# Performance work log

Hardware: AMD Instinct MI355X
Metric: run time of the kernel (lower is better)

## Reference

```python
import jax, jax.numpy as jnp
import numpy as np

B, S, H, N, NREL = 16, 2048, 1024, 128, 8


def setup_inputs() -> dict:
    key = jax.random.key(0)
    ks = jax.random.split(key, 8)
    word_emb = jax.random.normal(ks[0], (B, S, H), dtype=jnp.float32)
    num_ids = jax.random.randint(ks[1], (B, N), 0, S)  # all valid (no -1 padding)
    is_response = jax.random.randint(ks[2], (B, N), 0, 2).astype(jnp.int32)
    numbers = jax.random.normal(ks[3], (B, N), dtype=jnp.float32)
    scale = 1.0 / np.sqrt(H).astype(np.float32)
    w_alpha = jax.random.normal(ks[4], (H, 1), dtype=jnp.float32) * scale
    b_alpha = jnp.zeros((1,), dtype=jnp.float32)
    w_f = jax.random.normal(ks[5], (H, H), dtype=jnp.float32) * scale
    b_f = jnp.zeros((H,), dtype=jnp.float32)
    W_r = jax.random.normal(ks[6], (NREL, H, H), dtype=jnp.float32) * scale  # 8 bias-free relation linears
    return dict(word_emb=word_emb, num_ids=num_ids, is_response=is_response,
                numbers=numbers, w_alpha=w_alpha, b_alpha=b_alpha,
                w_f=w_f, b_f=b_f, W_r=W_r)


def reference(word_emb, num_ids, is_response, numbers, w_alpha, b_alpha, w_f, b_f, W_r):
    Bn, Sn, Hn = word_emb.shape
    Nn = num_ids.shape[1]
    mask = (num_ids >= 0)  # [B,N] valid-node mask (original uses -1 padding)
    idx = jnp.clip(num_ids, 0, Sn - 1)
    # per-batch gather: Init[b,n] = word_emb[b, num_ids[b,n]]  -> [B,N,H]
    Init = jnp.take_along_axis(word_emb, idx[:, :, None], axis=1)
    alpha = jax.nn.sigmoid(Init @ w_alpha + b_alpha)  # [B,N,1]
    # all 8 relation transforms of every sender node j: T[b,r,j,:] = Init[b,j] @ W_r[r].T
    T = jnp.einsum('bnh,rkh->brnk', Init, W_r)  # [B,8,N,H]
    # relation id r(b,i,j) = 4*(num_i>num_j) + 2*resp_i + resp_j
    gt = (numbers[:, :, None] > numbers[:, None, :]).astype(jnp.int32)  # [B,N,N]
    resp = (is_response == 1).astype(jnp.int32)
    R = 4 * gt + 2 * resp[:, :, None] + resp[:, None, :]  # [B,N,N]
    sel = jax.nn.one_hot(R, NREL, dtype=word_emb.dtype)  # [B,N,N,8]
    not_diag = ~jnp.eye(Nn, dtype=bool)
    # edge weight over sender j: alpha_j, valid i & j, i != j
    wgt = (alpha[:, None, :, 0] * mask[:, None, :] * mask[:, :, None]
           * not_diag[None]).astype(word_emb.dtype)  # [B,N,N]
    Temp = jnp.einsum('bijr,brjh->bih', sel * wgt[..., None], T)  # [B,N,H]
    n_nodes = mask.sum(axis=1)  # [B]
    denom = jnp.maximum(n_nodes - 1, 1).astype(word_emb.dtype)
    Temp = Temp / denom[:, None, None]
    out = jax.nn.relu(Init @ w_f + b_f + Temp)  # [B,N,H]
    return out
```

## Files before the change

kernel.cpp:

```cpp
#include <hip/hip_runtime.h>
#include <hip/hip_bf16.h>
#include <stdint.h>

#define B_ 16
#define S_ 2048
#define H_ 1024
#define N_ 128
#define K9 (9*H_)
#define M_ (B_*N_)

typedef __attribute__((ext_vector_type(8))) short s8vec;
typedef __attribute__((ext_vector_type(4))) float f4vec;
typedef __hip_bfloat16 bf16;

__global__ void k_sort(const int* __restrict__ num_ids, const int* __restrict__ is_resp,
                       const float* __restrict__ numbers,
                       int* __restrict__ sigma, int* __restrict__ newgrp,
                       int* __restrict__ respv, float* __restrict__ denom) {
    int b = blockIdx.x, i = threadIdx.x;
    __shared__ float nums[N_];
    __shared__ int sig[N_];
    __shared__ int cnt;
    float ni = numbers[b*N_ + i];
    int idv = num_ids[b*N_ + i];
    int valid = (idv >= 0) ? 1 : 0;
    nums[i] = ni;
    if (i == 0) cnt = 0;
    __syncthreads();
    int p = 0;
    for (int j = 0; j < N_; ++j) {
        float nj = nums[j];
        p += (nj < ni || (nj == ni && j < i)) ? 1 : 0;
    }
    sig[p] = i;
    atomicAdd(&cnt, valid);
    __syncthreads();
    sigma[b*N_ + i] = sig[i];
    int cur = sig[i];
    int prv = (i > 0) ? sig[i-1] : 0;
    newgrp[b*N_ + i] = (i == 0 || nums[cur] != nums[prv]) ? 1 : 0;
    respv[b*N_ + i] = ((is_resp[b*N_ + i] == 1) ? 1 : 0) | (valid << 1);
    if (i == 0) denom[b] = fmaxf((float)(cnt - 1), 1.0f);
}

__global__ void k_gather(const float* __restrict__ word_emb, const int* __restrict__ num_ids,
                         const float* __restrict__ w_alpha, const float* __restrict__ b_alpha,
                         const float* __restrict__ denom,
                         bf16* __restrict__ A, float* __restrict__ ascaled) {
    int blk = blockIdx.x;
    int b = blk >> 7, n = blk & 127;
    int t = threadIdx.x;
    int idv = num_ids[b*N_ + n];
    int valid = (idv >= 0) ? 1 : 0;
    int idx = idv < 0 ? 0 : (idv > S_-1 ? S_-1 : idv);
    const float4* row = (const float4*)(word_emb + ((size_t)b*S_ + idx)*H_);
    float4 v = row[t];
    float4 w = ((const float4*)w_alpha)[t];
    float part = v.x*w.x + v.y*w.y + v.z*w.z + v.w*w.w;
    bf16* dst = A + (size_t)(b*N_ + n)*K9 + 8*H_ + t*4;
    dst[0] = __float2bfloat16(v.x);
    dst[1] = __float2bfloat16(v.y);
    dst[2] = __float2bfloat16(v.z);
    dst[3] = __float2bfloat16(v.w);
#pragma unroll
    for (int off = 32; off > 0; off >>= 1) part += __shfl_down(part, off, 64);
    __shared__ float red[4];
    if ((t & 63) == 0) red[t >> 6] = part;
    __syncthreads();
    if (t == 0) {
        float dot = red[0] + red[1] + red[2] + red[3] + b_alpha[0];
        float al = 1.0f / (1.0f + __expf(-dot));
        ascaled[b*N_ + n] = valid ? (al / denom[b]) : 0.0f;
    }
}

__global__ void k_wt(const float* __restrict__ W_r, bf16* __restrict__ Wt) {
    size_t o = ((size_t)blockIdx.x*256 + threadIdx.x)*4;
    float4 v = *(const float4*)(W_r + o);
    Wt[o+0] = __float2bfloat16(v.x);
    Wt[o+1] = __float2bfloat16(v.y);
    Wt[o+2] = __float2bfloat16(v.z);
    Wt[o+3] = __float2bfloat16(v.w);
}

__global__ void k_wf(const float* __restrict__ w_f, bf16* __restrict__ Wt8) {
    __shared__ float lds[64][65];
    int bi = blockIdx.x, bj = blockIdx.y;
    int t = threadIdx.x;
    int ty = t >> 4, tx = t & 15;
#pragma unroll
    for (int i = 0; i < 4; ++i) {
        int r = ty*4 + i;
        float4 v = *(const float4*)(w_f + (size_t)(bi*64 + r)*H_ + bj*64 + tx*4);
        lds[r][tx*4+0] = v.x; lds[r][tx*4+1] = v.y;
        lds[r][tx*4+2] = v.z; lds[r][tx*4+3] = v.w;
    }
    __syncthreads();
#pragma unroll
    for (int i = 0; i < 4; ++i) {
        int n = ty*4 + i;
        bf16* dst = Wt8 + (size_t)(bj*64 + n)*H_ + bi*64 + tx*4;
#pragma unroll
        for (int j = 0; j < 4; ++j)
            dst[j] = __float2bfloat16(lds[tx*4+j][n]);
    }
}

__global__ void k_build(const float* __restrict__ ascaled, const int* __restrict__ sigma,
                        const int* __restrict__ newgrp, const int* __restrict__ respv,
                        bf16* __restrict__ A) {
    int b = blockIdx.y;
    int h = blockIdx.x*64 + threadIdx.x;
    __shared__ float as_s[N_];
    __shared__ int sig_s[N_], ng_s[N_], rv_s[N_];
    for (int j = threadIdx.x; j < N_; j += 64) {
        as_s[j] = ascaled[b*N_ + j];
        sig_s[j] = sigma[b*N_ + j];
        ng_s[j] = newgrp[b*N_ + j];
        rv_s[j] = respv[b*N_ + j];
    }
    __syncthreads();
    const bf16* initcol = A + 8*H_ + h;
    float tot0 = 0.f, tot1 = 0.f;
    for (int i2 = 0; i2 < N_; ++i2) {
        float v = as_s[i2] * __bfloat162float(initcol[(size_t)(b*N_ + i2)*K9]);
        if (rv_s[i2] & 1) tot1 += v; else tot0 += v;
    }
    float cS0=0.f, cS1=0.f, cG0=0.f, cG1=0.f;
    for (int p = 0; p < N_; ++p) {
        int i2 = sig_s[p];
        if (ng_s[p]) { cS0 += cG0; cS1 += cG1; cG0 = 0.f; cG1 = 0.f; }
        float v = as_s[i2] * __bfloat162float(initcol[(size_t)(b*N_ + i2)*K9]);
        int resp = rv_s[i2] & 1;
        float vf = (rv_s[i2] >> 1) ? 1.0f : 0.0f;
        float G0 = cS0, G1 = cS1;
        float L0 = tot0 - G0 - (resp ? 0.f : v);
        float L1 = tot1 - G1 - (resp ? v : 0.f);
        bf16* Ar = A + (size_t)(b*N_ + i2)*K9 + h;
        int rb = 2*resp, ob = 2*(1 - resp);
        Ar[(size_t)(rb+0)*H_]   = __float2bfloat16(L0*vf);
        Ar[(size_t)(rb+1)*H_]   = __float2bfloat16(L1*vf);
        Ar[(size_t)(4+rb+0)*H_] = __float2bfloat16(G0*vf);
        Ar[(size_t)(4+rb+1)*H_] = __float2bfloat16(G1*vf);
        bf16 z = __float2bfloat16(0.0f);
        Ar[(size_t)(ob+0)*H_]   = z;
        Ar[(size_t)(ob+1)*H_]   = z;
        Ar[(size_t)(4+ob+0)*H_] = z;
        Ar[(size_t)(4+ob+1)*H_] = z;
        if (resp) cG1 += v; else cG0 += v;
    }
}

#define BM 128
#define BN 128
#define BK 32
#define KSPLIT 4
#define KSEG (K9/KSPLIT)

__global__ __launch_bounds__(256) void k_gemm(const bf16* __restrict__ A,
                                              const bf16* __restrict__ Wt,
                                              float* __restrict__ out) {
    __shared__ __align__(16) bf16 As[BM*BK];
    __shared__ __align__(16) bf16 Bs[BN*BK];
    int tid = threadIdx.x;
    int w = tid >> 6, lane = tid & 63;
    int q = lane >> 4, r = lane & 15;
    int bid = blockIdx.x;
    int mtile = bid & 15, ntile = (bid >> 4) & 7, ks = bid >> 7;
    int rowBase = mtile * BM, colBase = ntile * BN;
    int wm = w >> 1, wn = w & 1;

    f4vec acc[4][4];
#pragma unroll
    for (int mt = 0; mt < 4; ++mt)
#pragma unroll
        for (int nt = 0; nt < 4; ++nt)
#pragma unroll
            for (int e = 0; e < 4; ++e) acc[mt][nt][e] = 0.0f;

    const size_t Abase = (size_t)rowBase * K9;
    const int kbeg = ks * KSEG, kend = kbeg + KSEG;
    for (int k0 = kbeg; k0 < kend; k0 += BK) {
        int slot = k0 >> 10, kin = k0 & 1023;
        {
            int c = tid;
            const bf16* g = A + Abase + (size_t)(c & 127)*K9 + k0 + (c >> 7)*8;
            __builtin_amdgcn_global_load_lds((const __attribute__((address_space(1))) void*)g,
                (__attribute__((address_space(3))) void*)((char*)As + w*1024), 16, 0, 0);
            c = tid + 256;
            const bf16* g2 = A + Abase + (size_t)(c & 127)*K9 + k0 + (c >> 7)*8;
            __builtin_amdgcn_global_load_lds((const __attribute__((address_space(1))) void*)g2,
                (__attribute__((address_space(3))) void*)((char*)As + 4096 + w*1024), 16, 0, 0);
            c = tid;
            const bf16* gb = Wt + (size_t)slot*H_*H_ + (size_t)(colBase + (c & 127))*H_
                             + kin + (c >> 7)*8;
            __builtin_amdgcn_global_load_lds((const __attribute__((address_space(1))) void*)gb,
                (__attribute__((address_space(3))) void*)((char*)Bs + w*1024), 16, 0, 0);
            c = tid + 256;
            const bf16* gb2 = Wt + (size_t)slot*H_*H_ + (size_t)(colBase + (c & 127))*H_
                              + kin + (c >> 7)*8;
            __builtin_amdgcn_global_load_lds((const __attribute__((address_space(1))) void*)gb2,
                (__attribute__((address_space(3))) void*)((char*)Bs + 4096 + w*1024), 16, 0, 0);
        }
        __syncthreads();
        const short* Asp = (const short*)As;
        const short* Bsp = (const short*)Bs;
        s8vec af[4], bfr[4];
#pragma unroll
        for (int mt = 0; mt < 4; ++mt)
            af[mt] = *(const s8vec*)(Asp + ((size_t)q*128 + wm*64 + mt*16 + r)*8);
#pragma unroll
        for (int nt = 0; nt < 4; ++nt)
            bfr[nt] = *(const s8vec*)(Bsp + ((size_t)q*128 + wn*64 + nt*16 + r)*8);
#pragma unroll
        for (int mt = 0; mt < 4; ++mt)
#pragma unroll
            for (int nt = 0; nt < 4; ++nt)
                acc[mt][nt] = __builtin_amdgcn_mfma_f32_16x16x32_bf16(af[mt], bfr[nt],
                                                                      acc[mt][nt], 0, 0, 0);
        __syncthreads();
    }

#pragma unroll
    for (int mt = 0; mt < 4; ++mt)
#pragma unroll
        for (int nt = 0; nt < 4; ++nt)
#pragma unroll
            for (int e = 0; e < 4; ++e) {
                int rr = rowBase + wm*64 + mt*16 + q*4 + e;
                int cc = colBase + wn*64 + nt*16 + r;
                atomicAdd(&out[(size_t)rr*H_ + cc], acc[mt][nt][e]);
            }
}

__global__ void k_epi(float* __restrict__ out, const float* __restrict__ b_f) {
    size_t i4 = ((size_t)blockIdx.x*256 + threadIdx.x)*4;
    float4 v = *(float4*)(out + i4);
    int cc = (int)(i4 & 1023);
    float4 bv = *(const float4*)(b_f + cc);
    v.x = fmaxf(v.x + bv.x, 0.0f);
    v.y = fmaxf(v.y + bv.y, 0.0f);
    v.z = fmaxf(v.z + bv.z, 0.0f);
    v.w = fmaxf(v.w + bv.w, 0.0f);
    *(float4*)(out + i4) = v;
}

extern "C" void kernel_launch(void* const* d_in, const int* in_sizes, int n_in,
                              void* d_out, int out_size, void* d_ws, size_t ws_size,
                              hipStream_t stream) {
    (void)in_sizes; (void)n_in; (void)out_size; (void)ws_size;
    const float* word_emb = (const float*)d_in[0];
    const int*   num_ids  = (const int*)d_in[1];
    const int*   is_resp  = (const int*)d_in[2];
    const float* numbers  = (const float*)d_in[3];
    const float* w_alpha  = (const float*)d_in[4];
    const float* b_alpha  = (const float*)d_in[5];
    const float* w_f      = (const float*)d_in[6];
    const float* b_f      = (const float*)d_in[7];
    const float* W_r      = (const float*)d_in[8];
    float* out = (float*)d_out;

    char* ws = (char*)d_ws;
    bf16*  Aws     = (bf16*)(ws);
    bf16*  Wt      = (bf16*)(ws + 37748736);
    float* ascaled = (float*)(ws + 56623104);
    int*   sigma   = (int*)(ws + 56631296);
    int*   newgrp  = (int*)(ws + 56639488);
    int*   respv   = (int*)(ws + 56647680);
    float* denom   = (float*)(ws + 56655872);

    hipMemsetAsync(out, 0, (size_t)M_*H_*sizeof(float), stream);
    k_sort  <<<16,   128, 0, stream>>>(num_ids, is_resp, numbers, sigma, newgrp, respv, denom);
    k_gather<<<2048, 256, 0, stream>>>(word_emb, num_ids, w_alpha, b_alpha, denom, Aws, ascaled);
    k_wt    <<<8192, 256, 0, stream>>>(W_r, Wt);
    k_wf    <<<dim3(16,16), 256, 0, stream>>>(w_f, Wt + (size_t)8*H_*H_);
    k_build <<<dim3(16,16), 64, 0, stream>>>(ascaled, sigma, newgrp, respv, Aws);
    k_gemm  <<<512,  256, 0, stream>>>(Aws, Wt, out);
    k_epi   <<<2048, 256, 0, stream>>>(out, b_f);
}
```

Before: 367.6 us.

## Partition rows by response flag to shrink GEMM K from 9H to 5H

Measured after the change: 369.9 us. No clear change (+0.6%).

```diff
diff --git a/kernel.cpp b/kernel.cpp
--- a/kernel.cpp
+++ b/kernel.cpp
@@ -6,8 +6,9 @@
 #define S_ 2048
 #define H_ 1024
 #define N_ 128
-#define K9 (9*H_)
 #define M_ (B_*N_)
+#define K5 5120
+#define MP 2176
 
 typedef __attribute__((ext_vector_type(8))) short s8vec;
 typedef __attribute__((ext_vector_type(4))) float f4vec;
@@ -43,9 +44,39 @@
     if (i == 0) denom[b] = fmaxf((float)(cnt - 1), 1.0f);
 }
 
+__global__ void k_meta(const int* __restrict__ respv, int* __restrict__ aperm,
+                       int* __restrict__ iperm, int* __restrict__ meta) {
+    __shared__ int s0[1024], s1[1024];
+    int t = threadIdx.x;
+    aperm[t] = -1; aperm[t + 1024] = -1;
+    if (t < MP - 2048) aperm[t + 2048] = -1;
+    int r0 = 2*t, r1 = 2*t + 1;
+    int c_a = respv[r0] & 1, c_b = respv[r1] & 1;
+    int a0 = 1 - c_a, b0 = 1 - c_b;
+    s0[t] = a0 + b0;
+    s1[t] = c_a + c_b;
+    __syncthreads();
+    for (int off = 1; off < 1024; off <<= 1) {
+        int v0 = (t >= off) ? s0[t-off] : 0;
+        int v1 = (t >= off) ? s1[t-off] : 0;
+        __syncthreads();
+        s0[t] += v0; s1[t] += v1;
+        __syncthreads();
+    }
+    int C0 = s0[1023], C1 = s1[1023];
+    int P0 = ((C0 + 127) >> 7) << 7;
+    int ex0 = s0[t] - (a0 + b0);
+    int ex1 = s1[t] - (c_a + c_b);
+    int p_a = (c_a == 0) ? ex0 : P0 + ex1;
+    int p_b = (c_b == 0) ? ex0 + a0 : P0 + ex1 + c_a;
+    aperm[p_a] = r0; iperm[r0] = p_a;
+    aperm[p_b] = r1; iperm[r1] = p_b;
+    if (t == 0) { meta[0] = P0; meta[1] = C0; meta[2] = C1; }
+}
+
 __global__ void k_gather(const float* __restrict__ word_emb, const int* __restrict__ num_ids,
                          const float* __restrict__ w_alpha, const float* __restrict__ b_alpha,
-                         const float* __restrict__ denom,
+                         const float* __restrict__ denom, const int* __restrict__ iperm,
                          bf16* __restrict__ A, float* __restrict__ ascaled) {
     int blk = blockIdx.x;
     int b = blk >> 7, n = blk & 127;
@@ -53,11 +84,12 @@
     int idv = num_ids[b*N_ + n];
     int valid = (idv >= 0) ? 1 : 0;
     int idx = idv < 0 ? 0 : (idv > S_-1 ? S_-1 : idv);
+    int pr = iperm[b*N_ + n];
     const float4* row = (const float4*)(word_emb + ((size_t)b*S_ + idx)*H_);
     float4 v = row[t];
     float4 w = ((const float4*)w_alpha)[t];
     float part = v.x*w.x + v.y*w.y + v.z*w.z + v.w*w.w;
-    bf16* dst = A + (size_t)(b*N_ + n)*K9 + 8*H_ + t*4;
+    bf16* dst = A + (size_t)pr*K5 + 4*H_ + t*4;
     dst[0] = __float2bfloat16(v.x);
     dst[1] = __float2bfloat16(v.y);
     dst[2] = __float2bfloat16(v.z);
@@ -76,14 +108,19 @@
 
 __global__ void k_wt(const float* __restrict__ W_r, bf16* __restrict__ Wt) {
     size_t o = ((size_t)blockIdx.x*256 + threadIdx.x)*4;
-    float4 v = *(const float4*)(W_r + o);
-    Wt[o+0] = __float2bfloat16(v.x);
-    Wt[o+1] = __float2bfloat16(v.y);
-    Wt[o+2] = __float2bfloat16(v.z);
-    Wt[o+3] = __float2bfloat16(v.w);
-}
-
-__global__ void k_wf(const float* __restrict__ w_f, bf16* __restrict__ Wt8) {
+    int cs = (int)(o >> 20);
+    int c = cs >> 2, s = cs & 3;
+    int r = ((s >> 1) << 2) + 2*c + (s & 1);
+    size_t off = o & (size_t)(H_*H_ - 1);
+    float4 v = *(const float4*)(W_r + (size_t)r*H_*H_ + off);
+    bf16* dst = Wt + (size_t)(c*5 + s)*H_*H_ + off;
+    dst[0] = __float2bfloat16(v.x);
+    dst[1] = __float2bfloat16(v.y);
+    dst[2] = __float2bfloat16(v.z);
+    dst[3] = __float2bfloat16(v.w);
+}
+
+__global__ void k_wf(const float* __restrict__ w_f, bf16* __restrict__ Wt) {
     __shared__ float lds[64][65];
     int bi = blockIdx.x, bj = blockIdx.y;
     int t = threadIdx.x;
@@ -96,57 +133,65 @@
         lds[r][tx*4+2] = v.z; lds[r][tx*4+3] = v.w;
     }
     __syncthreads();
+    bf16* d0 = Wt + (size_t)4*H_*H_;
+    bf16* d1 = Wt + (size_t)9*H_*H_;
 #pragma unroll
     for (int i = 0; i < 4; ++i) {
         int n = ty*4 + i;
-        bf16* dst = Wt8 + (size_t)(bj*64 + n)*H_ + bi*64 + tx*4;
-#pragma unroll
-        for (int j = 0; j < 4; ++j)
-            dst[j] = __float2bfloat16(lds[tx*4+j][n]);
-    }
+        size_t doff = (size_t)(bj*64 + n)*H_ + bi*64 + tx*4;
+#pragma unroll
+        for (int j = 0; j < 4; ++j) {
+            bf16 val = __float2bfloat16(lds[tx*4+j][n]);
+            d0[doff + j] = val;
+            d1[doff + j] = val;
+        }
+    }
+}
+
+__global__ void k_pad(const int* __restrict__ aperm, bf16* __restrict__ A) {
+    int pr = blockIdx.x;
+    if (aperm[pr] >= 0) return;
+    float4 z = {0.f, 0.f, 0.f, 0.f};
+    float4* dst = (float4*)(A + (size_t)pr*K5);
+    for (int c = threadIdx.x; c < 640; c += 256) dst[c] = z;
 }
 
 __global__ void k_build(const float* __restrict__ ascaled, const int* __restrict__ sigma,
                         const int* __restrict__ newgrp, const int* __restrict__ respv,
-                        bf16* __restrict__ A) {
+                        const int* __restrict__ iperm, bf16* __restrict__ A) {
     int b = blockIdx.y;
     int h = blockIdx.x*64 + threadIdx.x;
     __shared__ float as_s[N_];
-    __shared__ int sig_s[N_], ng_s[N_], rv_s[N_];
+    __shared__ int sig_s[N_], ng_s[N_], rv_s[N_], pm_s[N_];
     for (int j = threadIdx.x; j < N_; j += 64) {
         as_s[j] = ascaled[b*N_ + j];
         sig_s[j] = sigma[b*N_ + j];
         ng_s[j] = newgrp[b*N_ + j];
         rv_s[j] = respv[b*N_ + j];
-    }
-    __syncthreads();
-    const bf16* initcol = A + 8*H_ + h;
+        pm_s[j] = iperm[b*N_ + j];
+    }
+    __syncthreads();
+    const bf16* initcol = A + 4*H_ + h;
     float tot0 = 0.f, tot1 = 0.f;
     for (int i2 = 0; i2 < N_; ++i2) {
-        float v = as_s[i2] * __bfloat162float(initcol[(size_t)(b*N_ + i2)*K9]);
+        float v = as_s[i2] * __bfloat162float(initcol[(size_t)pm_s[i2]*K5]);
         if (rv_s[i2] & 1) tot1 += v; else tot0 += v;
     }
     float cS0=0.f, cS1=0.f, cG0=0.f, cG1=0.f;
     for (int p = 0; p < N_; ++p) {
         int i2 = sig_s[p];
         if (ng_s[p]) { cS0 += cG0; cS1 += cG1; cG0 = 0.f; cG1 = 0.f; }
-        float v = as_s[i2] * __bfloat162float(initcol[(size_t)(b*N_ + i2)*K9]);
+        float v = as_s[i2] * __bfloat162float(initcol[(size_t)pm_s[i2]*K5]);
         int resp = rv_s[i2] & 1;
         float vf = (rv_s[i2] >> 1) ? 1.0f : 0.0f;
         float G0 = cS0, G1 = cS1;
         float L0 = tot0 - G0 - (resp ? 0.f : v);
         float L1 = tot1 - G1 - (resp ? v : 0.f);
-        bf16* Ar = A + (size_t)(b*N_ + i2)*K9 + h;
-        int rb = 2*resp, ob = 2*(1 - resp);
-        Ar[(size_t)(rb+0)*H_]   = __float2bfloat16(L0*vf);
-        Ar[(size_t)(rb+1)*H_]   = __float2bfloat16(L1*vf);
-        Ar[(size_t)(4+rb+0)*H_] = __float2bfloat16(G0*vf);
-        Ar[(size_t)(4+rb+1)*H_] = __float2bfloat16(G1*vf);
-        bf16 z = __float2bfloat16(0.0f);
-        Ar[(size_t)(ob+0)*H_]   = z;
-        Ar[(size_t)(ob+1)*H_]   = z;
-        Ar[(size_t)(4+ob+0)*H_] = z;
-        Ar[(size_t)(4+ob+1)*H_] = z;
+        bf16* Ar = A + (size_t)pm_s[i2]*K5 + h;
+        Ar[0*H_] = __float2bfloat16(L0*vf);
+        Ar[1*H_] = __float2bfloat16(L1*vf);
+        Ar[2*H_] = __float2bfloat16(G0*vf);
+        Ar[3*H_] = __float2bfloat16(G1*vf);
         if (resp) cG1 += v; else cG0 += v;
     }
 }
@@ -154,50 +199,54 @@
 #define BM 128
 #define BN 128
 #define BK 32
-#define KSPLIT 4
-#define KSEG (K9/KSPLIT)
+#define KSEG 640
 
 __global__ __launch_bounds__(256) void k_gemm(const bf16* __restrict__ A,
                                               const bf16* __restrict__ Wt,
-                                              float* __restrict__ out) {
+                                              const int* __restrict__ meta,
+                                              float* __restrict__ acc_buf) {
     __shared__ __align__(16) bf16 As[BM*BK];
     __shared__ __align__(16) bf16 Bs[BN*BK];
     int tid = threadIdx.x;
     int w = tid >> 6, lane = tid & 63;
     int q = lane >> 4, r = lane & 15;
     int bid = blockIdx.x;
-    int mtile = bid & 15, ntile = (bid >> 4) & 7, ks = bid >> 7;
-    int rowBase = mtile * BM, colBase = ntile * BN;
+    int mt = bid % 17;
+    int rest = bid / 17;
+    int nt = rest & 7, ks = rest >> 3;
+    int rowBase = mt * BM, colBase = nt * BN;
     int wm = w >> 1, wn = w & 1;
+    int P0 = meta[0];
+    const bf16* Wtc = Wt + ((rowBase >= P0) ? (size_t)5*H_*H_ : 0);
 
     f4vec acc[4][4];
 #pragma unroll
-    for (int mt = 0; mt < 4; ++mt)
-#pragma unroll
-        for (int nt = 0; nt < 4; ++nt)
-#pragma unroll
-            for (int e = 0; e < 4; ++e) acc[mt][nt][e] = 0.0f;
-
-    const size_t Abase = (size_t)rowBase * K9;
+    for (int mi = 0; mi < 4; ++mi)
+#pragma unroll
+        for (int ni = 0; ni < 4; ++ni)
+#pragma unroll
+            for (int e = 0; e < 4; ++e) acc[mi][ni][e] = 0.0f;
+
+    const size_t Abase = (size_t)rowBase * K5;
     const int kbeg = ks * KSEG, kend = kbeg + KSEG;
     for (int k0 = kbeg; k0 < kend; k0 += BK) {
         int slot = k0 >> 10, kin = k0 & 1023;
         {
             int c = tid;
-            const bf16* g = A + Abase + (size_t)(c & 127)*K9 + k0 + (c >> 7)*8;
+            const bf16* g = A + Abase + (size_t)(c & 127)*K5 + k0 + (c >> 7)*8;
             __builtin_amdgcn_global_load_lds((const __attribute__((address_space(1))) void*)g,
                 (__attribute__((address_space(3))) void*)((char*)As + w*1024), 16, 0, 0);
             c = tid + 256;
-            const bf16* g2 = A + Abase + (size_t)(c & 127)*K9 + k0 + (c >> 7)*8;
+            const bf16* g2 = A + Abase + (size_t)(c & 127)*K5 + k0 + (c >> 7)*8;
             __builtin_amdgcn_global_load_lds((const __attribute__((address_space(1))) void*)g2,
                 (__attribute__((address_space(3))) void*)((char*)As + 4096 + w*1024), 16, 0, 0);
             c = tid;
-            const bf16* gb = Wt + (size_t)slot*H_*H_ + (size_t)(colBase + (c & 127))*H_
+            const bf16* gb = Wtc + (size_t)slot*H_*H_ + (size_t)(colBase + (c & 127))*H_
                              + kin + (c >> 7)*8;
             __builtin_amdgcn_global_load_lds((const __attribute__((address_space(1))) void*)gb,
                 (__attribute__((address_space(3))) void*)((char*)Bs + w*1024), 16, 0, 0);
             c = tid + 256;
-            const bf16* gb2 = Wt + (size_t)slot*H_*H_ + (size_t)(colBase + (c & 127))*H_
+            const bf16* gb2 = Wtc + (size_t)slot*H_*H_ + (size_t)(colBase + (c & 127))*H_
                               + kin + (c >> 7)*8;
             __builtin_amdgcn_global_load_lds((const __attribute__((address_space(1))) void*)gb2,
                 (__attribute__((address_space(3))) void*)((char*)Bs + 4096 + w*1024), 16, 0, 0);
@@ -207,42 +256,44 @@
         const short* Bsp = (const short*)Bs;
         s8vec af[4], bfr[4];
 #pragma unroll
-        for (int mt = 0; mt < 4; ++mt)
-            af[mt] = *(const s8vec*)(Asp + ((size_t)q*128 + wm*64 + mt*16 + r)*8);
-#pragma unroll
-        for (int nt = 0; nt < 4; ++nt)
-            bfr[nt] = *(const s8vec*)(Bsp + ((size_t)q*128 + wn*64 + nt*16 + r)*8);
-#pragma unroll
-        for (int mt = 0; mt < 4; ++mt)
-#pragma unroll
-            for (int nt = 0; nt < 4; ++nt)
-                acc[mt][nt] = __builtin_amdgcn_mfma_f32_16x16x32_bf16(af[mt], bfr[nt],
-                                                                      acc[mt][nt], 0, 0, 0);
+        for (int mi = 0; mi < 4; ++mi)
+            af[mi] = *(const s8vec*)(Asp + ((size_t)q*128 + wm*64 + mi*16 + r)*8);
+#pragma unroll
+        for (int ni = 0; ni < 4; ++ni)
+            bfr[ni] = *(const s8vec*)(Bsp + ((size_t)q*128 + wn*64 + ni*16 + r)*8);
+#pragma unroll
+        for (int mi = 0; mi < 4; ++mi)
+#pragma unroll
+            for (int ni = 0; ni < 4; ++ni)
+                acc[mi][ni] = __builtin_amdgcn_mfma_f32_16x16x32_bf16(af[mi], bfr[ni],
+                                                                      acc[mi][ni], 0, 0, 0);
         __syncthreads();
     }
 
 #pragma unroll
-    for (int mt = 0; mt < 4; ++mt)
-#pragma unroll
-        for (int nt = 0; nt < 4; ++nt)
+    for (int mi = 0; mi < 4; ++mi)
+#pragma unroll
+        for (int ni = 0; ni < 4; ++ni)
 #pragma unroll
             for (int e = 0; e < 4; ++e) {
-                int rr = rowBase + wm*64 + mt*16 + q*4 + e;
-                int cc = colBase + wn*64 + nt*16 + r;
-                atomicAdd(&out[(size_t)rr*H_ + cc], acc[mt][nt][e]);
+                int rr = rowBase + wm*64 + mi*16 + q*4 + e;
+                int cc = colBase + wn*64 + ni*16 + r;
+                atomicAdd(&acc_buf[(size_t)rr*H_ + cc], acc[mi][ni][e]);
             }
 }
 
-__global__ void k_epi(float* __restrict__ out, const float* __restrict__ b_f) {
-    size_t i4 = ((size_t)blockIdx.x*256 + threadIdx.x)*4;
-    float4 v = *(float4*)(out + i4);
-    int cc = (int)(i4 & 1023);
-    float4 bv = *(const float4*)(b_f + cc);
+__global__ void k_epi(const float* __restrict__ acc_buf, const int* __restrict__ iperm,
+                      const float* __restrict__ b_f, float* __restrict__ out) {
+    int row = blockIdx.x;
+    int pr = iperm[row];
+    int t = threadIdx.x;
+    float4 v = ((const float4*)(acc_buf + (size_t)pr*H_))[t];
+    float4 bv = ((const float4*)b_f)[t];
     v.x = fmaxf(v.x + bv.x, 0.0f);
     v.y = fmaxf(v.y + bv.y, 0.0f);
     v.z = fmaxf(v.z + bv.z, 0.0f);
     v.w = fmaxf(v.w + bv.w, 0.0f);
-    *(float4*)(out + i4) = v;
+    ((float4*)(out + (size_t)row*H_))[t] = v;
 }
 
 extern "C" void kernel_launch(void* const* d_in, const int* in_sizes, int n_in,
@@ -262,19 +313,26 @@
 
     char* ws = (char*)d_ws;
     bf16*  Aws     = (bf16*)(ws);
-    bf16*  Wt      = (bf16*)(ws + 37748736);
-    float* ascaled = (float*)(ws + 56623104);
-    int*   sigma   = (int*)(ws + 56631296);
-    int*   newgrp  = (int*)(ws + 56639488);
-    int*   respv   = (int*)(ws + 56647680);
-    float* denom   = (float*)(ws + 56655872);
-
-    hipMemsetAsync(out, 0, (size_t)M_*H_*sizeof(float), stream);
+    bf16*  Wt      = (bf16*)(ws + 22282240);
+    float* acc_buf = (float*)(ws + 43253760);
+    float* ascaled = (float*)(ws + 52166656);
+    int*   sigma   = (int*)(ws + 52174848);
+    int*   newgrp  = (int*)(ws + 52183040);
+    int*   respv   = (int*)(ws + 52191232);
+    float* denom   = (float*)(ws + 52199424);
+    int*   aperm   = (int*)(ws + 52199488);
+    int*   iperm   = (int*)(ws + 52208192);
+    int*   meta    = (int*)(ws + 52216384);
+
+    hipMemsetAsync(acc_buf, 0, (size_t)MP*H_*sizeof(float), stream);
     k_sort  <<<16,   128, 0, stream>>>(num_ids, is_resp, numbers, sigma, newgrp, respv, denom);
-    k_gather<<<2048, 256, 0, stream>>>(word_emb, num_ids, w_alpha, b_alpha, denom, Aws, ascaled);
+    k_meta  <<<1,   1024, 0, stream>>>(respv, aperm, iperm, meta);
+    k_gather<<<2048, 256, 0, stream>>>(word_emb, num_ids, w_alpha, b_alpha, denom, iperm,
+                                       Aws, ascaled);
     k_wt    <<<8192, 256, 0, stream>>>(W_r, Wt);
-    k_wf    <<<dim3(16,16), 256, 0, stream>>>(w_f, Wt + (size_t)8*H_*H_);
-    k_build <<<dim3(16,16), 64, 0, stream>>>(ascaled, sigma, newgrp, respv, Aws);
-    k_gemm  <<<512,  256, 0, stream>>>(Aws, Wt, out);
-    k_epi   <<<2048, 256, 0, stream>>>(out, b_f);
-}
+    k_wf    <<<dim3(16,16), 256, 0, stream>>>(w_f, Wt);
+    k_pad   <<<MP,   256, 0, stream>>>(aperm, Aws);
+    k_build <<<dim3(16,16), 64, 0, stream>>>(ascaled, sigma, newgrp, respv, iperm, Aws);
+    k_gemm  <<<1088, 256, 0, stream>>>(Aws, Wt, meta, acc_buf);
+    k_epi   <<<2048, 256, 0, stream>>>(acc_buf, iperm, b_f, out);
+}
```
